# Kernel tuning notes

Measured on AMD Instinct MI355X. Metric: run time of the kernel, lower is better.

## Reference

```python
import jax, jax.numpy as jnp
import numpy as np

B, C, L = 32, 4, 512


def setup_inputs() -> dict:
    key = jax.random.key(0)
    k1, k2, k3 = jax.random.split(key, 3)
    receptor = jax.random.normal(k1, (B, C, L, L), dtype=jnp.float32)
    ligand = jax.random.normal(k2, (B, C, L, L), dtype=jnp.float32)
    # per-sample integer translations in [-L//2, L//2)
    T = jax.random.randint(k3, (B, 2), -L // 2, L // 2).astype(jnp.int32)
    return {"receptor": receptor, "ligand": ligand, "T": T}


def _shift_mul_sum(v1, v2, dx, dy):
    # All four sign branches of the original reduce to:
    #   sum_{x,y,c} v1[c,x,y] * v2[c, x-dx, y-dy]   (zero outside bounds)
    Ld = v1.shape[-1]
    ix = jnp.arange(Ld) - dx            # source rows in v2
    iy = jnp.arange(Ld) - dy            # source cols in v2
    mx = (ix >= 0) & (ix < Ld)
    my = (iy >= 0) & (iy < Ld)
    ixc = jnp.clip(ix, 0, Ld - 1)
    iyc = jnp.clip(iy, 0, Ld - 1)
    v2s = v2[:, ixc[:, None], iyc[None, :]]            # [C, L, L] shifted
    mask = (mx[:, None] & my[None, :]).astype(v1.dtype)  # [L, L]
    return jnp.sum(v1 * v2s * mask, axis=(1, 2))       # [C]


def reference(receptor, ligand, T):
    # receptor, ligand: [B, C, L, L]; T: [B, 2] int -> output [B, C]
    return jax.vmap(_shift_mul_sum)(receptor, ligand, T[:, 0], T[:, 1])
```

## Files before the change

kernel.cpp:

```cpp
#include <hip/hip_runtime.h>

constexpr int B = 32;
constexpr int C = 4;
constexpr int L = 512;
constexpr int THREADS = 256;
constexpr int ROWS_PER_WAVE = 4;
constexpr int RPB = 4 * ROWS_PER_WAVE;
constexpr int CHUNKS = L / RPB;

__device__ inline float4 ld4u(const float* p) {
    float4 v;
    __builtin_memcpy(&v, p, sizeof(float4));
    return v;
}

__global__ __launch_bounds__(THREADS)
void imgmul_stage1(const float* __restrict__ receptor,
                   const float* __restrict__ ligand,
                   const int* __restrict__ T,
                   float* __restrict__ partials)
{
    const int chunk = blockIdx.x;
    const int bc    = blockIdx.y;
    const int b     = bc >> 2;
    const int dx = T[2 * b + 0];
    const int dy = T[2 * b + 1];

    const int x0 = dx > 0 ? dx : 0;
    const int x1 = (L + dx) < L ? (L + dx) : L;
    const int y0 = dy > 0 ? dy : 0;
    const int y1 = (L + dy) < L ? (L + dy) : L;
    const int W  = y1 - y0;

    const int rbase = chunk * RPB;

    if (rbase + RPB <= x0 || rbase >= x1) {
        if (threadIdx.x == 0) partials[bc * CHUNKS + chunk] = 0.0f;
        return;
    }

    const size_t plane = (size_t)bc * (L * L);
    const float* rec = receptor + plane;
    const float* lig = ligand + plane;

    const int wave = threadIdx.x >> 6;
    const int lane = threadIdx.x & 63;

    const int  yq0 = y0 + 4 * lane;
    const int  e2  = 256 + 4 * lane;
    const bool m0  = (e2 + 0) < W;
    const bool m1  = (e2 + 1) < W;
    const bool m2  = (e2 + 2) < W;
    const bool m3  = (e2 + 3) < W;
    const int  yq1 = m0 ? (y0 + e2) : y0;

    bool vrow[ROWS_PER_WAVE];
    const float* rrow[ROWS_PER_WAVE];
    const float* lrow[ROWS_PER_WAVE];
    #pragma unroll
    for (int r = 0; r < ROWS_PER_WAVE; ++r) {
        const int x  = rbase + wave + 4 * r;
        const bool v = (x >= x0) & (x < x1);
        vrow[r] = v;
        const int xc = v ? x : x0;
        rrow[r] = rec + (size_t)xc * L;
        lrow[r] = lig + (size_t)(xc - dx) * L - dy;
    }

    float4 rv0[ROWS_PER_WAVE], lv0[ROWS_PER_WAVE];
    float4 rv1[ROWS_PER_WAVE], lv1[ROWS_PER_WAVE];
    #pragma unroll
    for (int r = 0; r < ROWS_PER_WAVE; ++r) {
        rv0[r] = ld4u(rrow[r] + yq0);
        lv0[r] = ld4u(lrow[r] + yq0);
        rv1[r] = ld4u(rrow[r] + yq1);
        lv1[r] = ld4u(lrow[r] + yq1);
    }

    float acc = 0.0f;
    #pragma unroll
    for (int r = 0; r < ROWS_PER_WAVE; ++r) {
        float d0 = rv0[r].x * lv0[r].x;
        d0 = fmaf(rv0[r].y, lv0[r].y, d0);
        d0 = fmaf(rv0[r].z, lv0[r].z, d0);
        d0 = fmaf(rv0[r].w, lv0[r].w, d0);
        float d1 = (m0 ? rv1[r].x * lv1[r].x : 0.0f)
                 + (m1 ? rv1[r].y * lv1[r].y : 0.0f)
                 + (m2 ? rv1[r].z * lv1[r].z : 0.0f)
                 + (m3 ? rv1[r].w * lv1[r].w : 0.0f);
        acc += vrow[r] ? (d0 + d1) : 0.0f;
    }

    #pragma unroll
    for (int off = 32; off > 0; off >>= 1)
        acc += __shfl_down(acc, off, 64);

    __shared__ float wsum[THREADS / 64];
    if (lane == 0) wsum[wave] = acc;
    __syncthreads();

    if (threadIdx.x == 0)
        partials[bc * CHUNKS + chunk] = wsum[0] + wsum[1] + wsum[2] + wsum[3];
}

__global__ __launch_bounds__(64)
void imgmul_stage2(const float* __restrict__ partials, float* __restrict__ out)
{
    const int bc = blockIdx.x;
    const int lane = threadIdx.x & 63;
    float v = (lane < CHUNKS) ? partials[bc * CHUNKS + lane] : 0.0f;
    #pragma unroll
    for (int off = 32; off > 0; off >>= 1)
        v += __shfl_down(v, off, 64);
    if (lane == 0) out[bc] = v;
}

extern "C" void kernel_launch(void* const* d_in, const int* in_sizes, int n_in,
                              void* d_out, int out_size, void* d_ws, size_t ws_size,
                              hipStream_t stream)
{
    const float* receptor = (const float*)d_in[0];
    const float* ligand   = (const float*)d_in[1];
    const int*   T        = (const int*)d_in[2];
    float* out      = (float*)d_out;
    float* partials = (float*)d_ws;

    imgmul_stage1<<<dim3(CHUNKS, B * C), dim3(THREADS), 0, stream>>>(
        receptor, ligand, T, partials);
    imgmul_stage2<<<dim3(B * C), dim3(64), 0, stream>>>(partials, out);
}
```

Before: 32.66 us.

## Split only the valid overlap rows evenly across fewer blocks per plane

```diff
diff --git a/kernel.cpp b/kernel.cpp
--- a/kernel.cpp
+++ b/kernel.cpp
@@ -4,9 +4,7 @@
 constexpr int C = 4;
 constexpr int L = 512;
 constexpr int THREADS = 256;
-constexpr int ROWS_PER_WAVE = 4;
-constexpr int RPB = 4 * ROWS_PER_WAVE;
-constexpr int CHUNKS = L / RPB;
+constexpr int KSPLIT = 16;
 
 __device__ inline float4 ld4u(const float* p) {
     float4 v;
@@ -20,9 +18,9 @@
                    const int* __restrict__ T,
                    float* __restrict__ partials)
 {
-    const int chunk = blockIdx.x;
-    const int bc    = blockIdx.y;
-    const int b     = bc >> 2;
+    const int k  = blockIdx.x;
+    const int bc = blockIdx.y;
+    const int b  = bc >> 2;
     const int dx = T[2 * b + 0];
     const int dy = T[2 * b + 1];
 
@@ -31,13 +29,10 @@
     const int y0 = dy > 0 ? dy : 0;
     const int y1 = (L + dy) < L ? (L + dy) : L;
     const int W  = y1 - y0;
+    const int nv = x1 - x0;
 
-    const int rbase = chunk * RPB;
-
-    if (rbase + RPB <= x0 || rbase >= x1) {
-        if (threadIdx.x == 0) partials[bc * CHUNKS + chunk] = 0.0f;
-        return;
-    }
+    const int rb = x0 + (nv * k) / KSPLIT;
+    const int re = x0 + (nv * (k + 1)) / KSPLIT;
 
     const size_t plane = (size_t)bc * (L * L);
     const float* rec = receptor + plane;
@@ -54,41 +49,25 @@
     const bool m3  = (e2 + 3) < W;
     const int  yq1 = m0 ? (y0 + e2) : y0;
 
-    bool vrow[ROWS_PER_WAVE];
-    const float* rrow[ROWS_PER_WAVE];
-    const float* lrow[ROWS_PER_WAVE];
-    #pragma unroll
-    for (int r = 0; r < ROWS_PER_WAVE; ++r) {
-        const int x  = rbase + wave + 4 * r;
-        const bool v = (x >= x0) & (x < x1);
-        vrow[r] = v;
-        const int xc = v ? x : x0;
-        rrow[r] = rec + (size_t)xc * L;
-        lrow[r] = lig + (size_t)(xc - dx) * L - dy;
-    }
+    float acc = 0.0f;
+    for (int x = rb + wave; x < re; x += 4) {
+        const float* rrow = rec + (size_t)x * L;
+        const float* lrow = lig + (size_t)(x - dx) * L - dy;
 
-    float4 rv0[ROWS_PER_WAVE], lv0[ROWS_PER_WAVE];
-    float4 rv1[ROWS_PER_WAVE], lv1[ROWS_PER_WAVE];
-    #pragma unroll
-    for (int r = 0; r < ROWS_PER_WAVE; ++r) {
-        rv0[r] = ld4u(rrow[r] + yq0);
-        lv0[r] = ld4u(lrow[r] + yq0);
-        rv1[r] = ld4u(rrow[r] + yq1);
-        lv1[r] = ld4u(lrow[r] + yq1);
-    }
+        const float4 a0 = ld4u(rrow + yq0);
+        const float4 b0 = ld4u(lrow + yq0);
+        const float4 a1 = ld4u(rrow + yq1);
+        const float4 b1 = ld4u(lrow + yq1);
 
-    float acc = 0.0f;
-    #pragma unroll
-    for (int r = 0; r < ROWS_PER_WAVE; ++r) {
-        float d0 = rv0[r].x * lv0[r].x;
-        d0 = fmaf(rv0[r].y, lv0[r].y, d0);
-        d0 = fmaf(rv0[r].z, lv0[r].z, d0);
-        d0 = fmaf(rv0[r].w, lv0[r].w, d0);
-        float d1 = (m0 ? rv1[r].x * lv1[r].x : 0.0f)
-                 + (m1 ? rv1[r].y * lv1[r].y : 0.0f)
-                 + (m2 ? rv1[r].z * lv1[r].z : 0.0f)
-                 + (m3 ? rv1[r].w * lv1[r].w : 0.0f);
-        acc += vrow[r] ? (d0 + d1) : 0.0f;
+        float d = a0.x * b0.x;
+        d = fmaf(a0.y, b0.y, d);
+        d = fmaf(a0.z, b0.z, d);
+        d = fmaf(a0.w, b0.w, d);
+        d += (m0 ? a1.x * b1.x : 0.0f)
+           + (m1 ? a1.y * b1.y : 0.0f)
+           + (m2 ? a1.z * b1.z : 0.0f)
+           + (m3 ? a1.w * b1.w : 0.0f);
+        acc += d;
     }
 
     #pragma unroll
@@ -100,7 +79,7 @@
     __syncthreads();
 
     if (threadIdx.x == 0)
-        partials[bc * CHUNKS + chunk] = wsum[0] + wsum[1] + wsum[2] + wsum[3];
+        partials[bc * KSPLIT + k] = wsum[0] + wsum[1] + wsum[2] + wsum[3];
 }
 
 __global__ __launch_bounds__(64)
@@ -108,7 +87,7 @@
 {
     const int bc = blockIdx.x;
     const int lane = threadIdx.x & 63;
-    float v = (lane < CHUNKS) ? partials[bc * CHUNKS + lane] : 0.0f;
+    float v = (lane < KSPLIT) ? partials[bc * KSPLIT + lane] : 0.0f;
     #pragma unroll
     for (int off = 32; off > 0; off >>= 1)
         v += __shfl_down(v, off, 64);
@@ -125,7 +104,7 @@
     float* out      = (float*)d_out;
     float* partials = (float*)d_ws;
 
-    imgmul_stage1<<<dim3(CHUNKS, B * C), dim3(THREADS), 0, stream>>>(
+    imgmul_stage1<<<dim3(KSPLIT, B * C), dim3(THREADS), 0, stream>>>(
         receptor, ligand, T, partials);
     imgmul_stage2<<<dim3(B * C), dim3(64), 0, stream>>>(partials, out);
 }
```

New measurement: 33.01 us. Within noise of the previous version (+1.1%).
